# Performance work log

Hardware: AMD Instinct MI355X
Metric: run time of the kernel (lower is better)

The kernel has to match this reference:

```python
import jax, jax.numpy as jnp
import numpy as np

IN_F = 1024
OUT_F = 1024

def setup_inputs() -> dict:
    key = jax.random.key(0)
    ks = jax.random.split(key, 7)
    s = 1.0 / np.sqrt(IN_F)
    x = jax.random.normal(ks[0], (4, 2048, IN_F), dtype=jnp.float32)
    Wq = jax.random.uniform(ks[1], (OUT_F, IN_F), jnp.float32, -s, s)
    bq = jax.random.uniform(ks[2], (OUT_F,), jnp.float32, -s, s)
    Wk = jax.random.uniform(ks[3], (OUT_F, IN_F), jnp.float32, -s, s)
    bk = jax.random.uniform(ks[4], (OUT_F,), jnp.float32, -s, s)
    Wv = jax.random.uniform(ks[5], (OUT_F, IN_F), jnp.float32, -s, s)
    bv = jax.random.uniform(ks[6], (OUT_F,), jnp.float32, -s, s)
    return {"x": x, "Wq": Wq, "bq": bq, "Wk": Wk, "bk": bk, "Wv": Wv, "bv": bv}

def reference(x, Wq, bq, Wk, bk, Wv, bv):
    # Projector: ReLU(Linear(x))
    q = jax.nn.relu(jnp.einsum('bsd,od->bso', x, Wq) + bq)  # [B,S,O]
    k = jax.nn.relu(jnp.einsum('bsd,od->bso', x, Wk) + bk)
    v = jax.nn.relu(jnp.einsum('bsd,od->bso', x, Wv) + bv)
    logits = jnp.einsum('bio,bko->bik', q, k)  # unscaled QK^T, [B,S,S]
    scores = jax.nn.softmax(logits, axis=-1)
    out = jnp.einsum('bik,bko->bio', scores, v)
    return out
```

## Files before the change

kernel.cpp:

```cpp
#include <hip/hip_runtime.h>
#include <hip/hip_bf16.h>


#define SEQ 2048
#define DIM 1024
#define NB 4
#define MTOT (NB * SEQ)

typedef __attribute__((ext_vector_type(8))) short frag_ab;
typedef __attribute__((ext_vector_type(16))) float frag_c16;

__device__ __forceinline__ ushort f2bf(float f) {
    union { float f; unsigned u; } x; x.f = f;
    unsigned r = x.u + 0x7fffu + ((x.u >> 16) & 1u);
    return (ushort)(r >> 16);
}

typedef __attribute__((address_space(1))) const unsigned int guint;
typedef __attribute__((address_space(3))) unsigned int luint;

__device__ __forceinline__ void gld_lds16(const void* g, void* l) {
    __builtin_amdgcn_global_load_lds((guint*)g, (luint*)l, 16, 0, 0);
}

__device__ __forceinline__ void gemm_tiles(
    const ushort* __restrict__ A, size_t lda,
    const ushort* __restrict__ B, size_t ldb, int K,
    ushort* As, ushort* Bs, frag_c16 (&acc)[2][2])
{
    const int tid  = threadIdx.x;
    const int wave = tid >> 6;
    const int lane = tid & 63;
    const int l32  = lane & 31;
    const int half = lane >> 5;
    const int sr = wave * 16 + (lane >> 2);
    const int sc = lane & 3;
    const int wm = (wave & 1) * 64;
    const int wn = (wave >> 1) * 64;

    for (int k0 = 0; k0 < K; k0 += 32) {
        #pragma unroll
        for (int j = 0; j < 2; ++j) {
            int row = j * 64 + sr;
            int cg  = sc ^ ((row >> 1) & 3);
            ushort* la = As + (j * 64 + wave * 16) * 32;
            ushort* lb = Bs + (j * 64 + wave * 16) * 32;
            gld_lds16(A + (size_t)row * lda + k0 + cg * 8, la);
            gld_lds16(B + (size_t)row * ldb + k0 + cg * 8, lb);
        }
        __syncthreads();
        frag_ab af[2][2], bfr[2][2];
        #pragma unroll
        for (int mi = 0; mi < 2; ++mi) {
            int row = wm + mi * 32 + l32;
            int sw = (row >> 1) & 3;
            #pragma unroll
            for (int h = 0; h < 2; ++h) {
                int c = (h * 2 + half) ^ sw;
                af[mi][h] = *(const frag_ab*)&As[row * 32 + c * 8];
            }
        }
        #pragma unroll
        for (int ni = 0; ni < 2; ++ni) {
            int row = wn + ni * 32 + l32;
            int sw = (row >> 1) & 3;
            #pragma unroll
            for (int h = 0; h < 2; ++h) {
                int c = (h * 2 + half) ^ sw;
                bfr[ni][h] = *(const frag_ab*)&Bs[row * 32 + c * 8];
            }
        }
        #pragma unroll
        for (int h = 0; h < 2; ++h)
            #pragma unroll
            for (int mi = 0; mi < 2; ++mi)
                #pragma unroll
                for (int ni = 0; ni < 2; ++ni)
                    acc[mi][ni] = __builtin_amdgcn_mfma_f32_32x32x16_bf16(
                        af[mi][h], bfr[ni][h], acc[mi][ni], 0, 0, 0);
        __syncthreads();
    }
}


#define NX4 (MTOT * DIM / 4)
#define NW4 (DIM * DIM / 4)
__global__ __launch_bounds__(256) void cvt_kernel(
    const float* __restrict__ x,
    const float* __restrict__ Wq, const float* __restrict__ Wk,
    const float* __restrict__ Wv,
    ushort* __restrict__ xb, ushort* __restrict__ Wb)
{
    size_t i = (size_t)blockIdx.x * 256 + threadIdx.x;
    const float* src; ushort* dst; size_t idx;
    if (i < NX4) { src = x; dst = xb; idx = i; }
    else {
        size_t j = i - NX4;
        int w = (int)(j >> 18);
        idx = j & (NW4 - 1);
        src = w == 0 ? Wq : (w == 1 ? Wk : Wv);
        dst = Wb + (size_t)w * DIM * DIM;
    }
    float4 f = ((const float4*)src)[idx];
    ushort4 u; u.x = f2bf(f.x); u.y = f2bf(f.y); u.z = f2bf(f.z); u.w = f2bf(f.w);
    ((ushort4*)dst)[idx] = u;
}

__global__ __launch_bounds__(256) void qkv_kernel(
    const ushort* __restrict__ xb, const ushort* __restrict__ Wb,
    const float* __restrict__ bq, const float* __restrict__ bk,
    const float* __restrict__ bv,
    ushort* __restrict__ q, ushort* __restrict__ k, ushort* __restrict__ v)
{
    const float* bias; ushort* out;
    if (blockIdx.z == 0)      { bias = bq; out = q; }
    else if (blockIdx.z == 1) { bias = bk; out = k; }
    else                      { bias = bv; out = v; }
    const ushort* W = Wb + (size_t)blockIdx.z * DIM * DIM;

    __shared__ ushort As[128 * 32];
    __shared__ ushort Bs[128 * 32];

    const int tid  = threadIdx.x;
    const int wave = tid >> 6;
    const int lane = tid & 63;
    const int l32  = lane & 31;
    const int half = lane >> 5;
    const int m0 = blockIdx.x * 128;
    const int n0 = blockIdx.y * 128;
    const int wm = (wave & 1) * 64;
    const int wn = (wave >> 1) * 64;

    frag_c16 acc[2][2] = {};
    gemm_tiles(xb + (size_t)m0 * DIM, DIM, W + (size_t)n0 * DIM, DIM, DIM,
               As, Bs, acc);

    #pragma unroll
    for (int ni = 0; ni < 2; ++ni) {
        int col = n0 + wn + ni * 32 + l32;
        float bb = bias[col];
        #pragma unroll
        for (int mi = 0; mi < 2; ++mi)
            #pragma unroll
            for (int r = 0; r < 16; ++r) {
                int row = m0 + wm + mi * 32 + (r & 3) + 8 * (r >> 2) + 4 * half;
                float val = acc[mi][ni][r] + bb;
                val = val > 0.0f ? val : 0.0f;
                out[(size_t)row * DIM + col] = f2bf(val);
            }
    }
}

__global__ __launch_bounds__(256) void transpose_v(
    const ushort* __restrict__ v, ushort* __restrict__ vt)
{
    __shared__ ushort T[64][72];
    const int bz = blockIdx.z;
    const int s0 = blockIdx.x * 64;
    const int o0 = blockIdx.y * 64;
    const int t  = threadIdx.x;

    #pragma unroll
    for (int p = 0; p < 4; ++p) {
        int sl = p * 16 + (t >> 4);
        int o4 = (t & 15) * 4;
        ushort4 u = *(const ushort4*)&v[(size_t)(bz * SEQ + s0 + sl) * DIM + o0 + o4];
        *(ushort4*)&T[sl][o4] = u;
    }
    __syncthreads();
    #pragma unroll
    for (int p = 0; p < 4; ++p) {
        int ol = p * 16 + (t >> 4);
        int s4 = (t & 15) * 4;
        ushort4 u;
        u.x = T[s4 + 0][ol]; u.y = T[s4 + 1][ol];
        u.z = T[s4 + 2][ol]; u.w = T[s4 + 3][ol];
        *(ushort4*)&vt[(size_t)(bz * DIM + o0 + ol) * SEQ + s0 + s4] = u;
    }
}

__global__ __launch_bounds__(256) void qk_kernel(
    const ushort* __restrict__ q, const ushort* __restrict__ kk,
    float* __restrict__ logits)
{
    __shared__ ushort As[128 * 32];
    __shared__ ushort Bs[128 * 32];

    const int tid  = threadIdx.x;
    const int wave = tid >> 6;
    const int lane = tid & 63;
    const int l32  = lane & 31;
    const int half = lane >> 5;
    const int bz = blockIdx.z;
    const int m0 = blockIdx.x * 128;
    const int n0 = blockIdx.y * 128;
    const int wm = (wave & 1) * 64;
    const int wn = (wave >> 1) * 64;
    const size_t base = (size_t)bz * SEQ;

    frag_c16 acc[2][2] = {};
    gemm_tiles(q + (base + m0) * DIM, DIM, kk + (base + n0) * DIM, DIM, DIM,
               As, Bs, acc);

    #pragma unroll
    for (int mi = 0; mi < 2; ++mi)
        #pragma unroll
        for (int r = 0; r < 16; ++r) {
            int row = m0 + wm + mi * 32 + (r & 3) + 8 * (r >> 2) + 4 * half;
            #pragma unroll
            for (int ni = 0; ni < 2; ++ni) {
                int col = n0 + wn + ni * 32 + l32;
                logits[(base + row) * SEQ + col] = acc[mi][ni][r];
            }
        }
}

__global__ __launch_bounds__(256) void softmax_kernel(float* __restrict__ logits)
{
    float* p = logits + (size_t)blockIdx.x * SEQ;
    const int t = threadIdx.x;
    const int wave = t >> 6, lane = t & 63;

    float4 a = ((const float4*)p)[t];
    float4 b = ((const float4*)p)[t + 256];

    float m = fmaxf(fmaxf(fmaxf(a.x, a.y), fmaxf(a.z, a.w)),
                    fmaxf(fmaxf(b.x, b.y), fmaxf(b.z, b.w)));
    #pragma unroll
    for (int off = 32; off; off >>= 1) m = fmaxf(m, __shfl_down(m, off, 64));

    __shared__ float red[4];
    if (lane == 0) red[wave] = m;
    __syncthreads();
    m = fmaxf(fmaxf(red[0], red[1]), fmaxf(red[2], red[3]));

    a.x = __expf(a.x - m); a.y = __expf(a.y - m);
    a.z = __expf(a.z - m); a.w = __expf(a.w - m);
    b.x = __expf(b.x - m); b.y = __expf(b.y - m);
    b.z = __expf(b.z - m); b.w = __expf(b.w - m);

    float s = (a.x + a.y + a.z + a.w) + (b.x + b.y + b.z + b.w);
    #pragma unroll
    for (int off = 32; off; off >>= 1) s += __shfl_down(s, off, 64);
    __syncthreads();
    if (lane == 0) red[wave] = s;
    __syncthreads();
    s = red[0] + red[1] + red[2] + red[3];
    float inv = 1.0f / s;

    ushort* o = (ushort*)p;
    ushort4 u0, u1;
    u0.x = f2bf(a.x * inv); u0.y = f2bf(a.y * inv);
    u0.z = f2bf(a.z * inv); u0.w = f2bf(a.w * inv);
    u1.x = f2bf(b.x * inv); u1.y = f2bf(b.y * inv);
    u1.z = f2bf(b.z * inv); u1.w = f2bf(b.w * inv);
    ((ushort4*)o)[t]       = u0;
    ((ushort4*)o)[t + 256] = u1;
}

__global__ __launch_bounds__(256) void pv_kernel(
    const ushort* __restrict__ probs, const ushort* __restrict__ vt,
    float* __restrict__ out)
{
    __shared__ ushort As[128 * 32];
    __shared__ ushort Bs[128 * 32];

    const int tid  = threadIdx.x;
    const int wave = tid >> 6;
    const int lane = tid & 63;
    const int l32  = lane & 31;
    const int half = lane >> 5;
    const int bz = blockIdx.z;
    const int m0 = blockIdx.x * 128;
    const int n0 = blockIdx.y * 128;
    const int wm = (wave & 1) * 64;
    const int wn = (wave >> 1) * 64;

    frag_c16 acc[2][2] = {};
    gemm_tiles(probs + ((size_t)(bz * SEQ + m0)) * 4096, 4096,
               vt + ((size_t)(bz * DIM + n0)) * SEQ, SEQ, SEQ,
               As, Bs, acc);

    #pragma unroll
    for (int mi = 0; mi < 2; ++mi)
        #pragma unroll
        for (int r = 0; r < 16; ++r) {
            int row = m0 + wm + mi * 32 + (r & 3) + 8 * (r >> 2) + 4 * half;
            #pragma unroll
            for (int ni = 0; ni < 2; ++ni) {
                int col = n0 + wn + ni * 32 + l32;
                out[((size_t)(bz * SEQ + row)) * DIM + col] = acc[mi][ni][r];
            }
        }
}

extern "C" void kernel_launch(void* const* d_in, const int* in_sizes, int n_in,
                              void* d_out, int out_size, void* d_ws, size_t ws_size,
                              hipStream_t stream)
{
    const float* x  = (const float*)d_in[0];
    const float* Wq = (const float*)d_in[1];
    const float* bq = (const float*)d_in[2];
    const float* Wk = (const float*)d_in[3];
    const float* bk = (const float*)d_in[4];
    const float* Wv = (const float*)d_in[5];
    const float* bv = (const float*)d_in[6];
    float* out = (float*)d_out;

    char* ws = (char*)d_ws;
    ushort* q      = (ushort*)(ws);
    ushort* kk     = (ushort*)(ws + ((size_t)16 << 20));
    ushort* v      = (ushort*)(ws + ((size_t)32 << 20));
    ushort* vt     = (ushort*)(ws + ((size_t)48 << 20));
    float*  logits = (float*) (ws + ((size_t)64 << 20));
    ushort* xb     = (ushort*)(ws + ((size_t)64 << 20));
    ushort* Wb     = (ushort*)(ws + ((size_t)80 << 20));

    cvt_kernel<<<dim3((NX4 + 3 * NW4) / 256), 256, 0, stream>>>(
        x, Wq, Wk, Wv, xb, Wb);

    qkv_kernel<<<dim3(MTOT / 128, DIM / 128, 3), 256, 0, stream>>>(
        xb, Wb, bq, bk, bv, q, kk, v);
    transpose_v<<<dim3(SEQ / 64, DIM / 64, NB), 256, 0, stream>>>(v, vt);
    qk_kernel<<<dim3(SEQ / 128, SEQ / 128, NB), 256, 0, stream>>>(q, kk, logits);
    softmax_kernel<<<NB * SEQ, 256, 0, stream>>>(logits);
    pv_kernel<<<dim3(SEQ / 128, DIM / 128, NB), 256, 0, stream>>>(
        (const ushort*)logits, vt, out);
}
```

Baseline: 277.0 us.

## Double GEMM K-tile, fuse V transpose into QKV epilogue, use wave-per-row softmax

The shared GEMM loop now stages 64-wide K tiles instead of 32, with an 8-way XOR swizzle. This halves the number of barrier pairs per GEMM and doubles LDS use per block. The V projection epilogue writes directly in transposed layout, which removes the separate transpose kernel and its round trip through memory. Softmax now handles one row per wave using xor shuffles, with no shared-memory reductions or block barriers. The larger LDS footprint may lower occupancy.

```diff
diff --git a/kernel.cpp b/kernel.cpp
--- a/kernel.cpp
+++ b/kernel.cpp
@@ -33,51 +33,50 @@
     const int lane = tid & 63;
     const int l32  = lane & 31;
     const int half = lane >> 5;
-    const int sr = wave * 16 + (lane >> 2);
-    const int sc = lane & 3;
+    const int rin  = lane >> 3;
+    const int cp   = lane & 7;
+    const int cl   = cp ^ rin;
     const int wm = (wave & 1) * 64;
     const int wn = (wave >> 1) * 64;
 
-    for (int k0 = 0; k0 < K; k0 += 32) {
-        #pragma unroll
-        for (int j = 0; j < 2; ++j) {
-            int row = j * 64 + sr;
-            int cg  = sc ^ ((row >> 1) & 3);
-            ushort* la = As + (j * 64 + wave * 16) * 32;
-            ushort* lb = Bs + (j * 64 + wave * 16) * 32;
-            gld_lds16(A + (size_t)row * lda + k0 + cg * 8, la);
-            gld_lds16(B + (size_t)row * ldb + k0 + cg * 8, lb);
+    for (int k0 = 0; k0 < K; k0 += 64) {
+        #pragma unroll
+        for (int g = 0; g < 4; ++g) {
+            int qc  = g * 4 + wave;
+            int row = qc * 8 + rin;
+            gld_lds16(A + (size_t)row * lda + k0 + cl * 8, As + qc * 512);
+            gld_lds16(B + (size_t)row * ldb + k0 + cl * 8, Bs + qc * 512);
         }
         __syncthreads();
-        frag_ab af[2][2], bfr[2][2];
+        frag_ab af[2][4], bf[2][4];
         #pragma unroll
         for (int mi = 0; mi < 2; ++mi) {
             int row = wm + mi * 32 + l32;
-            int sw = (row >> 1) & 3;
-            #pragma unroll
-            for (int h = 0; h < 2; ++h) {
-                int c = (h * 2 + half) ^ sw;
-                af[mi][h] = *(const frag_ab*)&As[row * 32 + c * 8];
+            int sw = row & 7;
+            #pragma unroll
+            for (int ks = 0; ks < 4; ++ks) {
+                int c = (ks * 2 + half) ^ sw;
+                af[mi][ks] = *(const frag_ab*)&As[row * 64 + c * 8];
             }
         }
         #pragma unroll
         for (int ni = 0; ni < 2; ++ni) {
             int row = wn + ni * 32 + l32;
-            int sw = (row >> 1) & 3;
-            #pragma unroll
-            for (int h = 0; h < 2; ++h) {
-                int c = (h * 2 + half) ^ sw;
-                bfr[ni][h] = *(const frag_ab*)&Bs[row * 32 + c * 8];
+            int sw = row & 7;
+            #pragma unroll
+            for (int ks = 0; ks < 4; ++ks) {
+                int c = (ks * 2 + half) ^ sw;
+                bf[ni][ks] = *(const frag_ab*)&Bs[row * 64 + c * 8];
             }
         }
         #pragma unroll
-        for (int h = 0; h < 2; ++h)
+        for (int ks = 0; ks < 4; ++ks)
             #pragma unroll
             for (int mi = 0; mi < 2; ++mi)
                 #pragma unroll
                 for (int ni = 0; ni < 2; ++ni)
                     acc[mi][ni] = __builtin_amdgcn_mfma_f32_32x32x16_bf16(
-                        af[mi][h], bfr[ni][h], acc[mi][ni], 0, 0, 0);
+                        af[mi][ks], bf[ni][ks], acc[mi][ni], 0, 0, 0);
         __syncthreads();
     }
 }
@@ -110,16 +109,16 @@
     const ushort* __restrict__ xb, const ushort* __restrict__ Wb,
     const float* __restrict__ bq, const float* __restrict__ bk,
     const float* __restrict__ bv,
-    ushort* __restrict__ q, ushort* __restrict__ k, ushort* __restrict__ v)
-{
-    const float* bias; ushort* out;
-    if (blockIdx.z == 0)      { bias = bq; out = q; }
-    else if (blockIdx.z == 1) { bias = bk; out = k; }
-    else                      { bias = bv; out = v; }
+    ushort* __restrict__ q, ushort* __restrict__ kk, ushort* __restrict__ vt)
+{
+    const float* bias;
+    if (blockIdx.z == 0)      bias = bq;
+    else if (blockIdx.z == 1) bias = bk;
+    else                      bias = bv;
     const ushort* W = Wb + (size_t)blockIdx.z * DIM * DIM;
 
-    __shared__ ushort As[128 * 32];
-    __shared__ ushort Bs[128 * 32];
+    __shared__ ushort As[128 * 64];
+    __shared__ ushort Bs[128 * 64];
 
     const int tid  = threadIdx.x;
     const int wave = tid >> 6;
@@ -135,47 +134,45 @@
     gemm_tiles(xb + (size_t)m0 * DIM, DIM, W + (size_t)n0 * DIM, DIM, DIM,
                As, Bs, acc);
 
-    #pragma unroll
-    for (int ni = 0; ni < 2; ++ni) {
-        int col = n0 + wn + ni * 32 + l32;
-        float bb = bias[col];
-        #pragma unroll
-        for (int mi = 0; mi < 2; ++mi)
-            #pragma unroll
-            for (int r = 0; r < 16; ++r) {
-                int row = m0 + wm + mi * 32 + (r & 3) + 8 * (r >> 2) + 4 * half;
-                float val = acc[mi][ni][r] + bb;
-                val = val > 0.0f ? val : 0.0f;
-                out[(size_t)row * DIM + col] = f2bf(val);
-            }
-    }
-}
-
-__global__ __launch_bounds__(256) void transpose_v(
-    const ushort* __restrict__ v, ushort* __restrict__ vt)
-{
-    __shared__ ushort T[64][72];
-    const int bz = blockIdx.z;
-    const int s0 = blockIdx.x * 64;
-    const int o0 = blockIdx.y * 64;
-    const int t  = threadIdx.x;
-
-    #pragma unroll
-    for (int p = 0; p < 4; ++p) {
-        int sl = p * 16 + (t >> 4);
-        int o4 = (t & 15) * 4;
-        ushort4 u = *(const ushort4*)&v[(size_t)(bz * SEQ + s0 + sl) * DIM + o0 + o4];
-        *(ushort4*)&T[sl][o4] = u;
-    }
-    __syncthreads();
-    #pragma unroll
-    for (int p = 0; p < 4; ++p) {
-        int ol = p * 16 + (t >> 4);
-        int s4 = (t & 15) * 4;
-        ushort4 u;
-        u.x = T[s4 + 0][ol]; u.y = T[s4 + 1][ol];
-        u.z = T[s4 + 2][ol]; u.w = T[s4 + 3][ol];
-        *(ushort4*)&vt[(size_t)(bz * DIM + o0 + ol) * SEQ + s0 + s4] = u;
+    if (blockIdx.z == 2) {
+        const int bz = m0 >> 11;
+        const int sb = (m0 & (SEQ - 1)) + wm;
+        #pragma unroll
+        for (int ni = 0; ni < 2; ++ni) {
+            int col = n0 + wn + ni * 32 + l32;
+            float bb = bias[col];
+            ushort* vrow = vt + ((size_t)(bz * DIM + col)) * SEQ;
+            #pragma unroll
+            for (int mi = 0; mi < 2; ++mi)
+                #pragma unroll
+                for (int g = 0; g < 4; ++g) {
+                    int s0 = sb + mi * 32 + 8 * g + 4 * half;
+                    ushort4 u;
+                    #pragma unroll
+                    for (int j = 0; j < 4; ++j) {
+                        float val = acc[mi][ni][4 * g + j] + bb;
+                        val = val > 0.0f ? val : 0.0f;
+                        ((ushort*)&u)[j] = f2bf(val);
+                    }
+                    *(ushort4*)&vrow[s0] = u;
+                }
+        }
+    } else {
+        ushort* out = blockIdx.z == 0 ? q : kk;
+        #pragma unroll
+        for (int ni = 0; ni < 2; ++ni) {
+            int col = n0 + wn + ni * 32 + l32;
+            float bb = bias[col];
+            #pragma unroll
+            for (int mi = 0; mi < 2; ++mi)
+                #pragma unroll
+                for (int r = 0; r < 16; ++r) {
+                    int row = m0 + wm + mi * 32 + (r & 3) + 8 * (r >> 2) + 4 * half;
+                    float val = acc[mi][ni][r] + bb;
+                    val = val > 0.0f ? val : 0.0f;
+                    out[(size_t)row * DIM + col] = f2bf(val);
+                }
+        }
     }
 }
 
@@ -183,8 +180,8 @@
     const ushort* __restrict__ q, const ushort* __restrict__ kk,
     float* __restrict__ logits)
 {
-    __shared__ ushort As[128 * 32];
-    __shared__ ushort Bs[128 * 32];
+    __shared__ ushort As[128 * 64];
+    __shared__ ushort Bs[128 * 64];
 
     const int tid  = threadIdx.x;
     const int wave = tid >> 6;
@@ -217,53 +214,48 @@
 
 __global__ __launch_bounds__(256) void softmax_kernel(float* __restrict__ logits)
 {
-    float* p = logits + (size_t)blockIdx.x * SEQ;
-    const int t = threadIdx.x;
-    const int wave = t >> 6, lane = t & 63;
-
-    float4 a = ((const float4*)p)[t];
-    float4 b = ((const float4*)p)[t + 256];
-
-    float m = fmaxf(fmaxf(fmaxf(a.x, a.y), fmaxf(a.z, a.w)),
-                    fmaxf(fmaxf(b.x, b.y), fmaxf(b.z, b.w)));
-    #pragma unroll
-    for (int off = 32; off; off >>= 1) m = fmaxf(m, __shfl_down(m, off, 64));
-
-    __shared__ float red[4];
-    if (lane == 0) red[wave] = m;
-    __syncthreads();
-    m = fmaxf(fmaxf(red[0], red[1]), fmaxf(red[2], red[3]));
-
-    a.x = __expf(a.x - m); a.y = __expf(a.y - m);
-    a.z = __expf(a.z - m); a.w = __expf(a.w - m);
-    b.x = __expf(b.x - m); b.y = __expf(b.y - m);
-    b.z = __expf(b.z - m); b.w = __expf(b.w - m);
-
-    float s = (a.x + a.y + a.z + a.w) + (b.x + b.y + b.z + b.w);
-    #pragma unroll
-    for (int off = 32; off; off >>= 1) s += __shfl_down(s, off, 64);
-    __syncthreads();
-    if (lane == 0) red[wave] = s;
-    __syncthreads();
-    s = red[0] + red[1] + red[2] + red[3];
+    const int row  = blockIdx.x * 4 + (threadIdx.x >> 6);
+    const int lane = threadIdx.x & 63;
+    float* p = logits + (size_t)row * SEQ;
+
+    float4 x[8];
+    #pragma unroll
+    for (int i = 0; i < 8; ++i) x[i] = ((const float4*)p)[lane + 64 * i];
+
+    float m = -3.4e38f;
+    #pragma unroll
+    for (int i = 0; i < 8; ++i)
+        m = fmaxf(m, fmaxf(fmaxf(x[i].x, x[i].y), fmaxf(x[i].z, x[i].w)));
+    #pragma unroll
+    for (int off = 32; off; off >>= 1) m = fmaxf(m, __shfl_xor(m, off, 64));
+
+    float s = 0.0f;
+    #pragma unroll
+    for (int i = 0; i < 8; ++i) {
+        x[i].x = __expf(x[i].x - m); x[i].y = __expf(x[i].y - m);
+        x[i].z = __expf(x[i].z - m); x[i].w = __expf(x[i].w - m);
+        s += (x[i].x + x[i].y) + (x[i].z + x[i].w);
+    }
+    #pragma unroll
+    for (int off = 32; off; off >>= 1) s += __shfl_xor(s, off, 64);
     float inv = 1.0f / s;
 
     ushort* o = (ushort*)p;
-    ushort4 u0, u1;
-    u0.x = f2bf(a.x * inv); u0.y = f2bf(a.y * inv);
-    u0.z = f2bf(a.z * inv); u0.w = f2bf(a.w * inv);
-    u1.x = f2bf(b.x * inv); u1.y = f2bf(b.y * inv);
-    u1.z = f2bf(b.z * inv); u1.w = f2bf(b.w * inv);
-    ((ushort4*)o)[t]       = u0;
-    ((ushort4*)o)[t + 256] = u1;
+    #pragma unroll
+    for (int i = 0; i < 8; ++i) {
+        ushort4 u;
+        u.x = f2bf(x[i].x * inv); u.y = f2bf(x[i].y * inv);
+        u.z = f2bf(x[i].z * inv); u.w = f2bf(x[i].w * inv);
+        ((ushort4*)o)[lane + 64 * i] = u;
+    }
 }
 
 __global__ __launch_bounds__(256) void pv_kernel(
     const ushort* __restrict__ probs, const ushort* __restrict__ vt,
     float* __restrict__ out)
 {
-    __shared__ ushort As[128 * 32];
-    __shared__ ushort Bs[128 * 32];
+    __shared__ ushort As[128 * 64];
+    __shared__ ushort Bs[128 * 64];
 
     const int tid  = threadIdx.x;
     const int wave = tid >> 6;
@@ -310,7 +302,6 @@
     char* ws = (char*)d_ws;
     ushort* q      = (ushort*)(ws);
     ushort* kk     = (ushort*)(ws + ((size_t)16 << 20));
-    ushort* v      = (ushort*)(ws + ((size_t)32 << 20));
     ushort* vt     = (ushort*)(ws + ((size_t)48 << 20));
     float*  logits = (float*) (ws + ((size_t)64 << 20));
     ushort* xb     = (ushort*)(ws + ((size_t)64 << 20));
@@ -320,10 +311,9 @@
         x, Wq, Wk, Wv, xb, Wb);
 
     qkv_kernel<<<dim3(MTOT / 128, DIM / 128, 3), 256, 0, stream>>>(
-        xb, Wb, bq, bk, bv, q, kk, v);
-    transpose_v<<<dim3(SEQ / 64, DIM / 64, NB), 256, 0, stream>>>(v, vt);
+        xb, Wb, bq, bk, bv, q, kk, vt);
     qk_kernel<<<dim3(SEQ / 128, SEQ / 128, NB), 256, 0, stream>>>(q, kk, logits);
-    softmax_kernel<<<NB * SEQ, 256, 0, stream>>>(logits);
+    softmax_kernel<<<NB * SEQ / 4, 256, 0, stream>>>(logits);
     pv_kernel<<<dim3(SEQ / 128, DIM / 128, NB), 256, 0, stream>>>(
         (const ushort*)logits, vt, out);
 }
```

After: 265.3 us. -4.2%, faster.
